# Optimization experiments

Measured on AMD Instinct MI355X. Metric: run time of the kernel, lower is better.

The kernel has to match this reference:

```python
import jax, jax.numpy as jnp
import numpy as np
import math

DIM = 1024
HEADS = 16
DIM_HEAD = 64
INNER = HEADS * DIM_HEAD
NUM_BUCKETS = 32
MAX_DISTANCE = 128


def setup_inputs() -> dict:
    key = jax.random.key(0)
    ks = jax.random.split(key, 6)
    x = jax.random.normal(ks[0], (2, 2048, DIM), dtype=jnp.float32)
    Wq = jax.random.normal(ks[1], (DIM, INNER), dtype=jnp.float32) * (DIM ** -0.5)
    Wkv = jax.random.normal(ks[2], (DIM, 2 * DIM_HEAD), dtype=jnp.float32) * (DIM ** -0.5)
    Wout = jax.random.normal(ks[3], (INNER, DIM), dtype=jnp.float32) * (INNER ** -0.5)
    bout = jnp.zeros((DIM,), dtype=jnp.float32)
    rel_emb = jax.random.normal(ks[4], (NUM_BUCKETS, HEADS), dtype=jnp.float32) * 0.02
    return {"x": x, "Wq": Wq, "Wkv": Wkv, "Wout": Wout, "bout": bout, "rel_emb": rel_emb}


def _relative_position_bucket(rel_pos, num_buckets=NUM_BUCKETS, max_distance=MAX_DISTANCE):
    # rel_pos: [i, j] int32, k_pos - q_pos
    n = jnp.maximum(-rel_pos, 0)
    max_exact = num_buckets // 2
    is_small = n < max_exact
    n_safe = jnp.maximum(n, 1)  # avoid log(0); masked by is_small anyway
    val_if_large = max_exact + (
        jnp.log(n_safe.astype(jnp.float32) / max_exact)
        / math.log(max_distance / max_exact)
        * (num_buckets - max_exact)
    ).astype(jnp.int32)
    val_if_large = jnp.minimum(val_if_large, num_buckets - 1)
    return jnp.where(is_small, n, val_if_large)


def reference(x, Wq, Wkv, Wout, bout, rel_emb):
    b, n, _ = x.shape
    scale = DIM_HEAD ** -0.5
    bias_scale = DIM_HEAD ** 0.5

    q = (x @ Wq).reshape(b, n, HEADS, DIM_HEAD).transpose(0, 2, 1, 3) * scale  # [b,h,n,d]
    kv = x @ Wkv  # [b,n,2d]
    k, v = kv[..., :DIM_HEAD], kv[..., DIM_HEAD:]  # shared single-head K/V [b,n,d]

    sim = jnp.einsum('bhid,bjd->bhij', q, k)

    # T5 relative position bias
    pos = jnp.arange(n, dtype=jnp.int32)
    rel_pos = pos[None, :] - pos[:, None]  # [i,j] = k_pos - q_pos
    rp_bucket = _relative_position_bucket(rel_pos)
    bias = rel_emb[rp_bucket]  # [i,j,h]
    sim = sim + jnp.transpose(bias, (2, 0, 1))[None] * bias_scale

    # causal mask: mask strictly-upper triangle
    causal_mask = jnp.triu(jnp.ones((n, n), dtype=bool), k=1)
    neg = jnp.finfo(sim.dtype).max
    sim = jnp.where(causal_mask[None, None], -neg, sim)

    attn = jax.nn.softmax(sim, axis=-1)
    out = jnp.einsum('bhij,bjd->bhid', attn, v)
    out = out.transpose(0, 2, 1, 3).reshape(b, n, INNER)
    return out @ Wout + bout
```

## Files before the change

### kernel.cpp

```cpp
#include <hip/hip_runtime.h>
#include <cstdint>
#include <cmath>

typedef _Float16 half8 __attribute__((ext_vector_type(8)));
typedef unsigned short ushort8 __attribute__((ext_vector_type(8)));
typedef float floatx4 __attribute__((ext_vector_type(4)));

#define VT_STRIDE 2080

__device__ __forceinline__ unsigned short f2h(float f) {
    union { _Float16 h; unsigned short u; } cv;
    cv.h = (_Float16)f;
    return cv.u;
}

__device__ __forceinline__ void gld_lds16(const unsigned short* g, unsigned short* l) {
    __builtin_amdgcn_global_load_lds(
        (const __attribute__((address_space(1))) unsigned int*)g,
        (__attribute__((address_space(3))) unsigned int*)l, 16, 0, 0);
}

__global__ void prep_kernel(const float* __restrict__ x,
                            const float* __restrict__ Wq, const float* __restrict__ Wkv,
                            const float* __restrict__ Wout,
                            unsigned short* __restrict__ xh,
                            unsigned short* __restrict__ Wqkvt, unsigned short* __restrict__ Wot) {
    int bxi = blockIdx.x;
    if (bxi >= 68) {
        int fb = (bxi - 68) * 32 + blockIdx.y;
        int tt = threadIdx.y * 32 + threadIdx.x;
        int idx = fb * 256 + tt;
        const float4* p = (const float4*)x;
        float4 a = p[idx * 2], b = p[idx * 2 + 1];
        ushort8 o;
        o[0] = f2h(a.x); o[1] = f2h(a.y); o[2] = f2h(a.z); o[3] = f2h(a.w);
        o[4] = f2h(b.x); o[5] = f2h(b.y); o[6] = f2h(b.z); o[7] = f2h(b.w);
        *(ushort8*)(xh + (size_t)idx * 8) = o;
        return;
    }
    __shared__ float tile[32][33];
    const float* in; unsigned short* out; int C; int cb;
    if (bxi < 32)      { in = Wq;   out = Wqkvt;                 C = 1024; cb = bxi; }
    else if (bxi < 36) { in = Wkv;  out = Wqkvt + 1024 * 1024;   C = 128;  cb = bxi - 32; }
    else               { in = Wout; out = Wot;                   C = 1024; cb = bxi - 36; }
    int bx = cb * 32, by = blockIdx.y * 32;
    int xx = threadIdx.x, y0 = threadIdx.y;
    #pragma unroll
    for (int k = 0; k < 4; k++) {
        int y = y0 + k * 8;
        tile[y][xx] = in[(size_t)(by + y) * C + bx + xx];
    }
    __syncthreads();
    #pragma unroll
    for (int k = 0; k < 4; k++) {
        int y = y0 + k * 8;
        out[(size_t)(bx + y) * 1024 + by + xx] = f2h(tile[xx][y]);
    }
}

template<int MODE>
__global__ __launch_bounds__(256) void gemm_mn(
    const unsigned short* __restrict__ A, const unsigned short* __restrict__ Bt,
    unsigned short* __restrict__ oq, unsigned short* __restrict__ ok,
    unsigned short* __restrict__ ov, float* __restrict__ of,
    const float* __restrict__ bias)
{
    __shared__ __align__(16) unsigned short As[2][64 * 64];
    __shared__ __align__(16) unsigned short Bs[2][128 * 64];
    const int K = 1024;
    int t = threadIdx.x;
    int w = t >> 6, lane = t & 63, g = lane >> 4, il = lane & 15;
    int wr = w >> 1, wc = w & 1;
    int m0 = blockIdx.x * 64, n0 = blockIdx.y * 128;

    int l8 = lane >> 3, b8 = lane & 7;
    int swz = (b8 ^ l8) * 8;
    const unsigned short* Ag = A  + (size_t)(m0 + w * 16 + l8) * K + swz;
    const unsigned short* Bg = Bt + (size_t)(n0 + w * 32 + l8) * K + swz;
    int e0 = (g ^ (il & 7)) * 8;

    floatx4 acc[2][4] = {};

    #pragma unroll
    for (int q = 0; q < 2; q++)
        gld_lds16(Ag + (size_t)(q * 8) * K, &As[0][(w * 16 + q * 8) * 64]);
    #pragma unroll
    for (int q = 0; q < 4; q++)
        gld_lds16(Bg + (size_t)(q * 8) * K, &Bs[0][(w * 32 + q * 8) * 64]);

    int cb = 0;
    for (int k0 = 0; k0 < K; k0 += 64, cb ^= 1) {
        if (k0 + 64 < K) {
            #pragma unroll
            for (int q = 0; q < 2; q++)
                gld_lds16(Ag + (size_t)(q * 8) * K + k0 + 64, &As[cb ^ 1][(w * 16 + q * 8) * 64]);
            #pragma unroll
            for (int q = 0; q < 4; q++)
                gld_lds16(Bg + (size_t)(q * 8) * K + k0 + 64, &Bs[cb ^ 1][(w * 32 + q * 8) * 64]);
            asm volatile("s_waitcnt vmcnt(6)" ::: "memory");
        } else {
            asm volatile("s_waitcnt vmcnt(0)" ::: "memory");
        }
        __builtin_amdgcn_s_barrier();
        __builtin_amdgcn_sched_barrier(0);

        const unsigned short* Ac = &As[cb][0];
        const unsigned short* Bc = &Bs[cb][0];
        #pragma unroll
        for (int ks = 0; ks < 2; ks++) {
            half8 a[2];
            #pragma unroll
            for (int mt = 0; mt < 2; mt++)
                a[mt] = *(const half8*)&Ac[(wr * 32 + mt * 16 + il) * 64 + (e0 ^ (ks * 32))];
            #pragma unroll
            for (int nt = 0; nt < 4; nt++) {
                half8 b = *(const half8*)&Bc[(wc * 64 + nt * 16 + il) * 64 + (e0 ^ (ks * 32))];
                #pragma unroll
                for (int mt = 0; mt < 2; mt++)
                    acc[mt][nt] = __builtin_amdgcn_mfma_f32_16x16x32_f16(a[mt], b, acc[mt][nt], 0, 0, 0);
            }
        }
        asm volatile("s_waitcnt lgkmcnt(0)" ::: "memory");
        __builtin_amdgcn_s_barrier();
    }

    #pragma unroll
    for (int mt = 0; mt < 2; mt++) {
        #pragma unroll
        for (int nt = 0; nt < 4; nt++) {
            #pragma unroll
            for (int r = 0; r < 4; r++) {
                int row = m0 + wr * 32 + mt * 16 + 4 * g + r;
                int col = n0 + wc * 64 + nt * 16 + il;
                float v = acc[mt][nt][r];
                if (MODE == 0) {
                    if (col < 1024) {
                        int b = row >> 11, i = row & 2047, h = col >> 6, d = col & 63;
                        oq[(size_t)((b * 16 + h) * 2048 + i) * 64 + d] = f2h(v * 0.18033688011112042f);
                    } else if (col < 1088) {
                        ok[(size_t)row * 64 + (col - 1024)] = f2h(v);
                    } else {
                        int b = row >> 11, j = row & 2047;
                        ov[(size_t)((b << 6) + (col - 1088)) * VT_STRIDE + j] = f2h(v);
                    }
                } else {
                    of[(size_t)row * 1024 + col] = v + bias[col];
                }
            }
        }
    }
}

__global__ __launch_bounds__(256) void attn_kernel(
    const unsigned short* __restrict__ qh, const unsigned short* __restrict__ kh,
    const unsigned short* __restrict__ vt, const float* __restrict__ rel_emb,
    unsigned short* __restrict__ ob)
{
    __shared__ float bias_tab[256];
    __shared__ __align__(16) unsigned short Ks[64 * 64];
    __shared__ __align__(16) unsigned short Vs[64 * 64];
    __shared__ __align__(16) unsigned short Pl[64 * 72];

    int yy = blockIdx.y;
    int jp = yy & 7, sp = yy >> 3;
    int bx = (sp == 0) ? (31 - jp) : (sp == 1) ? jp : (sp == 2) ? (23 - jp) : (8 + jp);
    int bh = blockIdx.x;
    int b = bh >> 4, h = bh & 15;
    int t = threadIdx.x;
    int w = t >> 6, lane = t & 63, g = lane >> 4, il = lane & 15;

    {
        int dlt = t;
        int bucket;
        if (dlt < 16) bucket = dlt;
        else {
            float lg = logf((float)dlt * 0.0625f) / 2.0794415416798357f;
            int vv = 16 + (int)(lg * 16.0f);
            bucket = vv < 31 ? vv : 31;
        }
        bias_tab[dlt] = rel_emb[bucket * 16 + h] * 11.541560327111708f;
    }
    float cb31 = rel_emb[31 * 16 + h] * 11.541560327111708f;

    const unsigned short* kbase = kh + (size_t)b * (2048 * 64);
    const unsigned short* vbase = vt + (size_t)b * (64 * VT_STRIDE);
    int prow = (w * 16 + il) * 72;

    int l8 = lane >> 3, b8 = lane & 7;
    int swz = (b8 ^ l8) * 8;
    const unsigned short* kg_base = kbase + (size_t)(w * 16 + l8) * 64 + swz;
    const unsigned short* vg_base = vbase + (size_t)(w * 16 + l8) * VT_STRIDE + swz;
    int e0 = (g ^ (il & 7)) * 8;

    int iw = bx * 64 + w * 16;
    int i_glob = iw + il;
    const unsigned short* qrow = qh + (size_t)(bh * 2048 + i_glob) * 64;
    half8 qf0 = *(const half8*)(qrow + g * 8);
    half8 qf1 = *(const half8*)(qrow + 32 + g * 8);
    floatx4 O[4] = {};
    float m_run = -1e30f, l_run = 0.0f;

    gld_lds16(kg_base,                 &Ks[(w * 16) * 64]);
    gld_lds16(kg_base + 8 * 64,        &Ks[(w * 16 + 8) * 64]);
    gld_lds16(vg_base,                 &Vs[(w * 16) * 64]);
    gld_lds16(vg_base + 8 * VT_STRIDE, &Vs[(w * 16 + 8) * 64]);

    for (int c = 0; c <= bx; c++) {
        __syncthreads();
        int j0 = c * 64;

        floatx4 S[4] = {};
        #pragma unroll
        for (int jt = 0; jt < 4; jt++) {
            half8 k0 = *(const half8*)&Ks[jt * 1024 + il * 64 + e0];
            half8 k1 = *(const half8*)&Ks[jt * 1024 + il * 64 + (e0 ^ 32)];
            S[jt] = __builtin_amdgcn_mfma_f32_16x16x32_f16(k0, qf0, S[jt], 0, 0, 0);
            S[jt] = __builtin_amdgcn_mfma_f32_16x16x32_f16(k1, qf1, S[jt], 0, 0, 0);
        }
        half8 vf[8];
        #pragma unroll
        for (int ks = 0; ks < 2; ks++)
            #pragma unroll
            for (int dt = 0; dt < 4; dt++)
                vf[ks * 4 + dt] = *(const half8*)&Vs[dt * 1024 + il * 64 + (e0 ^ (ks * 32))];

        asm volatile("s_waitcnt lgkmcnt(0)" ::: "memory");
        __builtin_amdgcn_s_barrier();
        if (c < bx) {
            const unsigned short* kg = kg_base + (size_t)(c + 1) * 4096;
            const unsigned short* vg = vg_base + (c + 1) * 64;
            gld_lds16(kg,                 &Ks[(w * 16) * 64]);
            gld_lds16(kg + 8 * 64,        &Ks[(w * 16 + 8) * 64]);
            gld_lds16(vg,                 &Vs[(w * 16) * 64]);
            gld_lds16(vg + 8 * VT_STRIDE, &Vs[(w * 16 + 8) * 64]);
        }

        float s[16];
        if (c + 3 <= bx) {
            #pragma unroll
            for (int q2 = 0; q2 < 16; q2++) s[q2] = S[q2 >> 2][q2 & 3] + cb31;
        } else if (c < bx) {
            #pragma unroll
            for (int jt = 0; jt < 4; jt++)
                #pragma unroll
                for (int r = 0; r < 4; r++)
                    s[jt * 4 + r] = S[jt][r] + bias_tab[i_glob - (j0 + jt * 16 + 4 * g + r)];
        } else {
            #pragma unroll
            for (int jt = 0; jt < 4; jt++) {
                #pragma unroll
                for (int r = 0; r < 4; r++) {
                    int delta = i_glob - (j0 + jt * 16 + 4 * g + r);
                    int di = delta > 0 ? delta : 0;
                    s[jt * 4 + r] = (delta >= 0) ? (S[jt][r] + bias_tab[di]) : -1e30f;
                }
            }
        }
        float m8[8];
        #pragma unroll
        for (int q2 = 0; q2 < 8; q2++) m8[q2] = fmaxf(s[q2], s[q2 + 8]);
        #pragma unroll
        for (int q2 = 0; q2 < 4; q2++) m8[q2] = fmaxf(m8[q2], m8[q2 + 4]);
        float mx = fmaxf(fmaxf(m8[0], m8[1]), fmaxf(m8[2], m8[3]));
        mx = fmaxf(mx, __shfl_xor(mx, 16));
        mx = fmaxf(mx, __shfl_xor(mx, 32));
        float m_new = fmaxf(m_run, mx);
        float alpha = __builtin_amdgcn_exp2f(m_run - m_new);
        float p[16];
        #pragma unroll
        for (int q2 = 0; q2 < 16; q2++) p[q2] = __builtin_amdgcn_exp2f(s[q2] - m_new);
        float ps[8];
        #pragma unroll
        for (int q2 = 0; q2 < 8; q2++) ps[q2] = p[q2] + p[q2 + 8];
        #pragma unroll
        for (int q2 = 0; q2 < 4; q2++) ps[q2] += ps[q2 + 4];
        float psum = (ps[0] + ps[1]) + (ps[2] + ps[3]);
        psum += __shfl_xor(psum, 16);
        psum += __shfl_xor(psum, 32);
        l_run = l_run * alpha + psum;
        m_run = m_new;
        float arow[4];
        #pragma unroll
        for (int r = 0; r < 4; r++) arow[r] = __shfl(alpha, 4 * g + r);
        #pragma unroll
        for (int dt = 0; dt < 4; dt++)
            #pragma unroll
            for (int r = 0; r < 4; r++) O[dt][r] *= arow[r];

        #pragma unroll
        for (int jt = 0; jt < 4; jt++) {
            uint2 u;
            u.x = (unsigned int)f2h(p[jt * 4 + 0]) | ((unsigned int)f2h(p[jt * 4 + 1]) << 16);
            u.y = (unsigned int)f2h(p[jt * 4 + 2]) | ((unsigned int)f2h(p[jt * 4 + 3]) << 16);
            *(uint2*)&Pl[prow + jt * 16 + 4 * g] = u;
        }
        #pragma unroll
        for (int ks = 0; ks < 2; ks++) {
            half8 pf = *(const half8*)&Pl[prow + ks * 32 + g * 8];
            #pragma unroll
            for (int dt = 0; dt < 4; dt++)
                O[dt] = __builtin_amdgcn_mfma_f32_16x16x32_f16(pf, vf[ks * 4 + dt], O[dt], 0, 0, 0);
        }
    }
    float inv[4];
    #pragma unroll
    for (int r = 0; r < 4; r++) inv[r] = 1.0f / __shfl(l_run, 4 * g + r);
    #pragma unroll
    for (int dt = 0; dt < 4; dt++) {
        #pragma unroll
        for (int r = 0; r < 4; r++) {
            int i = iw + 4 * g + r;
            int d = dt * 16 + il;
            ob[(size_t)(b * 2048 + i) * 1024 + h * 64 + d] = f2h(O[dt][r] * inv[r]);
        }
    }
}

extern "C" void kernel_launch(void* const* d_in, const int* in_sizes, int n_in,
                              void* d_out, int out_size, void* d_ws, size_t ws_size,
                              hipStream_t stream) {
    const float* x    = (const float*)d_in[0];
    const float* Wq   = (const float*)d_in[1];
    const float* Wkv  = (const float*)d_in[2];
    const float* Wout = (const float*)d_in[3];
    const float* bout = (const float*)d_in[4];
    const float* rel  = (const float*)d_in[5];
    float* out = (float*)d_out;

    unsigned short* ws    = (unsigned short*)d_ws;
    unsigned short* xh    = ws;
    unsigned short* qh    = xh + 4194304;
    unsigned short* kh    = qh + 4194304;
    unsigned short* vt    = kh + 262144;
    unsigned short* Wqkvt = vt + 2 * 64 * VT_STRIDE;
    unsigned short* Wot   = Wqkvt + 1179648;
    unsigned short* ob    = xh;

    prep_kernel<<<dim3(132, 32), dim3(32, 8), 0, stream>>>(x, Wq, Wkv, Wout, xh, Wqkvt, Wot);
    gemm_mn<0><<<dim3(64, 9), 256, 0, stream>>>(xh, Wqkvt, qh, kh, vt, nullptr, nullptr);
    attn_kernel<<<dim3(32, 32), 256, 0, stream>>>(qh, kh, vt, rel, ob);
    gemm_mn<2><<<dim3(64, 8), 256, 0, stream>>>(ob, Wot, nullptr, nullptr, nullptr, out, bout);
}
```

Measured before the change: 159.3 us.

## Enlarge attention query tile to 128 rows with 8 warps sharing K/V tiles

The attention kernel now uses 512 threads per block, covering 128 query rows instead of 64, so each K/V tile loaded into LDS is reused by twice as many warps. Each warp loads half as much of the tile, and warps whose rows lie entirely before a key chunk skip the compute for it. The grid is halved and the block ordering is changed to pair long and short causal rows. The cost is more idle warps on the diagonal chunks, coarser load balance, and possible register pressure from the 512-thread launch bound.

After: 160.4 us. About the same (+0.7%).

```diff
diff --git a/kernel.cpp b/kernel.cpp
--- a/kernel.cpp
+++ b/kernel.cpp
@@ -151,7 +151,7 @@
     }
 }
 
-__global__ __launch_bounds__(256) void attn_kernel(
+__global__ __launch_bounds__(512) void attn_kernel(
     const unsigned short* __restrict__ qh, const unsigned short* __restrict__ kh,
     const unsigned short* __restrict__ vt, const float* __restrict__ rel_emb,
     unsigned short* __restrict__ ob)
@@ -159,17 +159,16 @@
     __shared__ float bias_tab[256];
     __shared__ __align__(16) unsigned short Ks[64 * 64];
     __shared__ __align__(16) unsigned short Vs[64 * 64];
-    __shared__ __align__(16) unsigned short Pl[64 * 72];
+    __shared__ __align__(16) unsigned short Pl[128 * 72];
 
     int yy = blockIdx.y;
-    int jp = yy & 7, sp = yy >> 3;
-    int bx = (sp == 0) ? (31 - jp) : (sp == 1) ? jp : (sp == 2) ? (23 - jp) : (8 + jp);
+    int bx = (yy < 8) ? (15 - 2 * yy) : (2 * (yy - 8));
     int bh = blockIdx.x;
     int b = bh >> 4, h = bh & 15;
     int t = threadIdx.x;
     int w = t >> 6, lane = t & 63, g = lane >> 4, il = lane & 15;
 
-    {
+    if (t < 256) {
         int dlt = t;
         int bucket;
         if (dlt < 16) bucket = dlt;
@@ -188,11 +187,11 @@
 
     int l8 = lane >> 3, b8 = lane & 7;
     int swz = (b8 ^ l8) * 8;
-    const unsigned short* kg_base = kbase + (size_t)(w * 16 + l8) * 64 + swz;
-    const unsigned short* vg_base = vbase + (size_t)(w * 16 + l8) * VT_STRIDE + swz;
+    const unsigned short* kg_base = kbase + (size_t)(w * 8 + l8) * 64 + swz;
+    const unsigned short* vg_base = vbase + (size_t)(w * 8 + l8) * VT_STRIDE + swz;
     int e0 = (g ^ (il & 7)) * 8;
 
-    int iw = bx * 64 + w * 16;
+    int iw = bx * 128 + w * 16;
     int i_glob = iw + il;
     const unsigned short* qrow = qh + (size_t)(bh * 2048 + i_glob) * 64;
     half8 qf0 = *(const half8*)(qrow + g * 8);
@@ -200,106 +199,107 @@
     floatx4 O[4] = {};
     float m_run = -1e30f, l_run = 0.0f;
 
-    gld_lds16(kg_base,                 &Ks[(w * 16) * 64]);
-    gld_lds16(kg_base + 8 * 64,        &Ks[(w * 16 + 8) * 64]);
-    gld_lds16(vg_base,                 &Vs[(w * 16) * 64]);
-    gld_lds16(vg_base + 8 * VT_STRIDE, &Vs[(w * 16 + 8) * 64]);
-
-    for (int c = 0; c <= bx; c++) {
+    gld_lds16(kg_base, &Ks[(w * 8) * 64]);
+    gld_lds16(vg_base, &Vs[(w * 8) * 64]);
+
+    int nc = 2 * bx + 1;
+    for (int c = 0; c <= nc; c++) {
         __syncthreads();
         int j0 = c * 64;
+        int d0 = iw - j0;
+        bool active = (d0 >= 0);
 
         floatx4 S[4] = {};
-        #pragma unroll
-        for (int jt = 0; jt < 4; jt++) {
-            half8 k0 = *(const half8*)&Ks[jt * 1024 + il * 64 + e0];
-            half8 k1 = *(const half8*)&Ks[jt * 1024 + il * 64 + (e0 ^ 32)];
-            S[jt] = __builtin_amdgcn_mfma_f32_16x16x32_f16(k0, qf0, S[jt], 0, 0, 0);
-            S[jt] = __builtin_amdgcn_mfma_f32_16x16x32_f16(k1, qf1, S[jt], 0, 0, 0);
-        }
         half8 vf[8];
-        #pragma unroll
-        for (int ks = 0; ks < 2; ks++)
-            #pragma unroll
-            for (int dt = 0; dt < 4; dt++)
-                vf[ks * 4 + dt] = *(const half8*)&Vs[dt * 1024 + il * 64 + (e0 ^ (ks * 32))];
+        if (active) {
+            #pragma unroll
+            for (int jt = 0; jt < 4; jt++) {
+                half8 k0 = *(const half8*)&Ks[jt * 1024 + il * 64 + e0];
+                half8 k1 = *(const half8*)&Ks[jt * 1024 + il * 64 + (e0 ^ 32)];
+                S[jt] = __builtin_amdgcn_mfma_f32_16x16x32_f16(k0, qf0, S[jt], 0, 0, 0);
+                S[jt] = __builtin_amdgcn_mfma_f32_16x16x32_f16(k1, qf1, S[jt], 0, 0, 0);
+            }
+            #pragma unroll
+            for (int ks = 0; ks < 2; ks++)
+                #pragma unroll
+                for (int dt = 0; dt < 4; dt++)
+                    vf[ks * 4 + dt] = *(const half8*)&Vs[dt * 1024 + il * 64 + (e0 ^ (ks * 32))];
+        }
 
         asm volatile("s_waitcnt lgkmcnt(0)" ::: "memory");
         __builtin_amdgcn_s_barrier();
-        if (c < bx) {
-            const unsigned short* kg = kg_base + (size_t)(c + 1) * 4096;
-            const unsigned short* vg = vg_base + (c + 1) * 64;
-            gld_lds16(kg,                 &Ks[(w * 16) * 64]);
-            gld_lds16(kg + 8 * 64,        &Ks[(w * 16 + 8) * 64]);
-            gld_lds16(vg,                 &Vs[(w * 16) * 64]);
-            gld_lds16(vg + 8 * VT_STRIDE, &Vs[(w * 16 + 8) * 64]);
-        }
-
-        float s[16];
-        if (c + 3 <= bx) {
-            #pragma unroll
-            for (int q2 = 0; q2 < 16; q2++) s[q2] = S[q2 >> 2][q2 & 3] + cb31;
-        } else if (c < bx) {
-            #pragma unroll
-            for (int jt = 0; jt < 4; jt++)
-                #pragma unroll
-                for (int r = 0; r < 4; r++)
-                    s[jt * 4 + r] = S[jt][r] + bias_tab[i_glob - (j0 + jt * 16 + 4 * g + r)];
-        } else {
+        if (c < nc) {
+            gld_lds16(kg_base + (size_t)(c + 1) * 4096, &Ks[(w * 8) * 64]);
+            gld_lds16(vg_base + (c + 1) * 64,           &Vs[(w * 8) * 64]);
+        }
+
+        if (active) {
+            float s[16];
+            if (d0 >= 176) {
+                #pragma unroll
+                for (int q2 = 0; q2 < 16; q2++) s[q2] = S[q2 >> 2][q2 & 3] + cb31;
+            } else if (d0 >= 64) {
+                #pragma unroll
+                for (int jt = 0; jt < 4; jt++)
+                    #pragma unroll
+                    for (int r = 0; r < 4; r++)
+                        s[jt * 4 + r] = S[jt][r] + bias_tab[i_glob - (j0 + jt * 16 + 4 * g + r)];
+            } else {
+                #pragma unroll
+                for (int jt = 0; jt < 4; jt++) {
+                    #pragma unroll
+                    for (int r = 0; r < 4; r++) {
+                        int delta = i_glob - (j0 + jt * 16 + 4 * g + r);
+                        int di = delta > 0 ? delta : 0;
+                        s[jt * 4 + r] = (delta >= 0) ? (S[jt][r] + bias_tab[di]) : -1e30f;
+                    }
+                }
+            }
+            float m8[8];
+            #pragma unroll
+            for (int q2 = 0; q2 < 8; q2++) m8[q2] = fmaxf(s[q2], s[q2 + 8]);
+            #pragma unroll
+            for (int q2 = 0; q2 < 4; q2++) m8[q2] = fmaxf(m8[q2], m8[q2 + 4]);
+            float mx = fmaxf(fmaxf(m8[0], m8[1]), fmaxf(m8[2], m8[3]));
+            mx = fmaxf(mx, __shfl_xor(mx, 16));
+            mx = fmaxf(mx, __shfl_xor(mx, 32));
+            float m_new = fmaxf(m_run, mx);
+            float alpha = __builtin_amdgcn_exp2f(m_run - m_new);
+            float p[16];
+            #pragma unroll
+            for (int q2 = 0; q2 < 16; q2++) p[q2] = __builtin_amdgcn_exp2f(s[q2] - m_new);
+            float ps[8];
+            #pragma unroll
+            for (int q2 = 0; q2 < 8; q2++) ps[q2] = p[q2] + p[q2 + 8];
+            #pragma unroll
+            for (int q2 = 0; q2 < 4; q2++) ps[q2] += ps[q2 + 4];
+            float psum = (ps[0] + ps[1]) + (ps[2] + ps[3]);
+            psum += __shfl_xor(psum, 16);
+            psum += __shfl_xor(psum, 32);
+            l_run = l_run * alpha + psum;
+            m_run = m_new;
+            float arow[4];
+            #pragma unroll
+            for (int r = 0; r < 4; r++) arow[r] = __shfl(alpha, 4 * g + r);
+            #pragma unroll
+            for (int dt = 0; dt < 4; dt++)
+                #pragma unroll
+                for (int r = 0; r < 4; r++) O[dt][r] *= arow[r];
+
             #pragma unroll
             for (int jt = 0; jt < 4; jt++) {
-                #pragma unroll
-                for (int r = 0; r < 4; r++) {
-                    int delta = i_glob - (j0 + jt * 16 + 4 * g + r);
-                    int di = delta > 0 ? delta : 0;
-                    s[jt * 4 + r] = (delta >= 0) ? (S[jt][r] + bias_tab[di]) : -1e30f;
-                }
-            }
-        }
-        float m8[8];
-        #pragma unroll
-        for (int q2 = 0; q2 < 8; q2++) m8[q2] = fmaxf(s[q2], s[q2 + 8]);
-        #pragma unroll
-        for (int q2 = 0; q2 < 4; q2++) m8[q2] = fmaxf(m8[q2], m8[q2 + 4]);
-        float mx = fmaxf(fmaxf(m8[0], m8[1]), fmaxf(m8[2], m8[3]));
-        mx = fmaxf(mx, __shfl_xor(mx, 16));
-        mx = fmaxf(mx, __shfl_xor(mx, 32));
-        float m_new = fmaxf(m_run, mx);
-        float alpha = __builtin_amdgcn_exp2f(m_run - m_new);
-        float p[16];
-        #pragma unroll
-        for (int q2 = 0; q2 < 16; q2++) p[q2] = __builtin_amdgcn_exp2f(s[q2] - m_new);
-        float ps[8];
-        #pragma unroll
-        for (int q2 = 0; q2 < 8; q2++) ps[q2] = p[q2] + p[q2 + 8];
-        #pragma unroll
-        for (int q2 = 0; q2 < 4; q2++) ps[q2] += ps[q2 + 4];
-        float psum = (ps[0] + ps[1]) + (ps[2] + ps[3]);
-        psum += __shfl_xor(psum, 16);
-        psum += __shfl_xor(psum, 32);
-        l_run = l_run * alpha + psum;
-        m_run = m_new;
-        float arow[4];
-        #pragma unroll
-        for (int r = 0; r < 4; r++) arow[r] = __shfl(alpha, 4 * g + r);
-        #pragma unroll
-        for (int dt = 0; dt < 4; dt++)
-            #pragma unroll
-            for (int r = 0; r < 4; r++) O[dt][r] *= arow[r];
-
-        #pragma unroll
-        for (int jt = 0; jt < 4; jt++) {
-            uint2 u;
-            u.x = (unsigned int)f2h(p[jt * 4 + 0]) | ((unsigned int)f2h(p[jt * 4 + 1]) << 16);
-            u.y = (unsigned int)f2h(p[jt * 4 + 2]) | ((unsigned int)f2h(p[jt * 4 + 3]) << 16);
-            *(uint2*)&Pl[prow + jt * 16 + 4 * g] = u;
-        }
-        #pragma unroll
-        for (int ks = 0; ks < 2; ks++) {
-            half8 pf = *(const half8*)&Pl[prow + ks * 32 + g * 8];
-            #pragma unroll
-            for (int dt = 0; dt < 4; dt++)
-                O[dt] = __builtin_amdgcn_mfma_f32_16x16x32_f16(pf, vf[ks * 4 + dt], O[dt], 0, 0, 0);
+                uint2 u;
+                u.x = (unsigned int)f2h(p[jt * 4 + 0]) | ((unsigned int)f2h(p[jt * 4 + 1]) << 16);
+                u.y = (unsigned int)f2h(p[jt * 4 + 2]) | ((unsigned int)f2h(p[jt * 4 + 3]) << 16);
+                *(uint2*)&Pl[prow + jt * 16 + 4 * g] = u;
+            }
+            #pragma unroll
+            for (int ks = 0; ks < 2; ks++) {
+                half8 pf = *(const half8*)&Pl[prow + ks * 32 + g * 8];
+                #pragma unroll
+                for (int dt = 0; dt < 4; dt++)
+                    O[dt] = __builtin_amdgcn_mfma_f32_16x16x32_f16(pf, vf[ks * 4 + dt], O[dt], 0, 0, 0);
+            }
         }
     }
     float inv[4];
@@ -338,6 +338,6 @@
 
     prep_kernel<<<dim3(132, 32), dim3(32, 8), 0, stream>>>(x, Wq, Wkv, Wout, xh, Wqkvt, Wot);
     gemm_mn<0><<<dim3(64, 9), 256, 0, stream>>>(xh, Wqkvt, qh, kh, vt, nullptr, nullptr);
-    attn_kernel<<<dim3(32, 32), 256, 0, stream>>>(qh, kh, vt, rel, ob);
+    attn_kernel<<<dim3(32, 16), dim3(512), 0, stream>>>(qh, kh, vt, rel, ob);
     gemm_mn<2><<<dim3(64, 8), 256, 0, stream>>>(ob, Wot, nullptr, nullptr, nullptr, out, bout);
 }
```
